# Kernel tuning notes

Hardware: AMD Instinct MI355X
Metric: run time of the kernel (lower is better)

Reference implementation:

```python
import jax, jax.numpy as jnp
import numpy as np


def _knn_idx(pts, k):
    # pts: [N, d] -> indices of k nearest neighbors (incl. self, loop=True) [N, k]
    sq = jnp.sum(pts * pts, axis=-1)
    d2 = sq[:, None] + sq[None, :] - 2.0 * (pts @ pts.T)  # [N, N] squared dists
    _, idx = jax.lax.top_k(-d2, k)  # k smallest distances
    return idx


def _graph_conv(x, nbr, Wr, br, Ws):
    # x: [B, N, d_in], nbr: [B, N, k]. GraphConv (aggr='add'):
    # out_i = W_rel @ sum_j x_j + b_rel + W_root @ x_i
    gathered = jax.vmap(lambda xb, ib: xb[ib])(x, nbr)  # [B, N, k, d_in]
    agg = gathered.sum(axis=2)                          # [B, N, d_in]
    return agg @ Wr.T + br + x @ Ws.T


def setup_inputs() -> dict:
    key = jax.random.key(0)
    ks = jax.random.split(key, 10)
    B, N, D, H = 16, 2048, 3, 128
    s = lambda fi, fo: (2.0 / (fi + fo)) ** 0.5
    return {
        "point_cloud": jax.random.normal(ks[0], (B, N, D), dtype=jnp.float32),
        "W1r": jax.random.normal(ks[1], (H, D), dtype=jnp.float32) * s(D, H),
        "b1": jnp.zeros((H,), dtype=jnp.float32),
        "W1s": jax.random.normal(ks[2], (H, D), dtype=jnp.float32) * s(D, H),
        "W2r": jax.random.normal(ks[3], (H, H), dtype=jnp.float32) * s(H, H),
        "b2": jnp.zeros((H,), dtype=jnp.float32),
        "W2s": jax.random.normal(ks[4], (H, H), dtype=jnp.float32) * s(H, H),
        "W3r": jax.random.normal(ks[5], (H, H), dtype=jnp.float32) * s(H, H),
        "b3": jnp.zeros((H,), dtype=jnp.float32),
        "W3s": jax.random.normal(ks[6], (H, H), dtype=jnp.float32) * s(H, H),
        "k": 16,
    }


def reference(point_cloud, W1r, b1, W1s, W2r, b2, W2s, W3r, b3, W3s, k):
    # knn graph per batch element (loop=True: self-loop included, d(i,i)=0)
    nbr = jax.vmap(lambda p: _knn_idx(p, k))(point_cloud)  # [B, N, k]
    x = jax.nn.relu(_graph_conv(point_cloud, nbr, W1r, b1, W1s))
    x = jax.nn.relu(_graph_conv(x, nbr, W2r, b2, W2s))
    x = _graph_conv(x, nbr, W3r, b3, W3s)
    return x  # [B, N, output_dim]
```

## Files before the change

### kernel.cpp

```cpp
#include <hip/hip_runtime.h>
#include <math.h>

#define NPTS 2048
#define BATCH 16
#define KNN 16
#define HID 128
#define NPOINTS (BATCH * NPTS)
#define RPB 8
#define CAP 64
#define KNN_BLOCKS (NPOINTS / RPB)

typedef __attribute__((ext_vector_type(8))) short bf16x8;
typedef __attribute__((ext_vector_type(4))) float f32x4;

__device__ inline unsigned short f2bf(float f) {
    unsigned u = __float_as_uint(f);
    return (unsigned short)((u + 0x7FFFu + ((u >> 16) & 1u)) >> 16);
}
__device__ inline float bflo(unsigned v) { return __uint_as_float(v << 16); }
__device__ inline float bfhi(unsigned v) { return __uint_as_float(v & 0xFFFF0000u); }


__global__ __launch_bounds__(512) void knn_kernel(
    const float* __restrict__ pc, int* __restrict__ nbr,
    const float* __restrict__ W1r, const float* __restrict__ b1,
    const float* __restrict__ W1s, unsigned short* __restrict__ x1,
    const float* __restrict__ W2r, const float* __restrict__ W2s,
    const float* __restrict__ W3r, const float* __restrict__ W3s,
    unsigned short* __restrict__ wT)
{
    __shared__ __align__(16) float4 pts[NPTS];
    __shared__ unsigned ckey[RPB][CAP];
    __shared__ unsigned cidx[RPB][CAP];
    __shared__ __align__(16) unsigned short xst[RPB][HID];

    if (blockIdx.x >= KNN_BLOCKS) {
        int g = (blockIdx.x - KNN_BLOCKS) * 2048 + (int)threadIdx.x * 4;
        #pragma unroll
        for (int u = 0; u < 4; ++u) {
            int g2 = g + u;
            int mm = g2 >> 14;
            int e = g2 & 16383;
            int r = e >> 7, cch = e & 127;
            const float* s = (mm == 0) ? W2r : (mm == 1) ? W2s
                           : (mm == 2) ? W3r : W3s;
            wT[mm * 16384 + ((cch >> 3) * 128 + r) * 8 + (cch & 7)] = f2bf(s[e]);
        }
        return;
    }

    const int b = blockIdx.x >> 8;
    const int rblk = blockIdx.x & 255;
    const float* p = pc + (size_t)b * NPTS * 3;

    for (int t = threadIdx.x; t < NPTS; t += 512) {
        float x = p[t * 3 + 0], y = p[t * 3 + 1], z = p[t * 3 + 2];
        pts[t] = make_float4(x, y, z, x * x + y * y + z * z);
    }
    __syncthreads();

    const int w = threadIdx.x >> 6;
    const int lane = threadIdx.x & 63;
    const int i = rblk * RPB + w;
    const float4 pi = pts[i];
    const float piw16 = pi.w + 16.0f;

    unsigned key[32];
    unsigned km = 0xFFFFFFFFu;
    #pragma unroll
    for (int t = 0; t < 32; ++t) {
        float4 c = pts[t * 64 + lane];
        float dot = fmaf(pi.x, c.x, fmaf(pi.y, c.y, pi.z * c.z));
        float d2 = fmaf(-2.0f, dot, piw16 + c.w);
        key[t] = __float_as_uint(d2);
        km = min(km, key[t]);
    }

    unsigned v = km;
    #pragma unroll
    for (int k = 2; k <= 64; k <<= 1) {
        #pragma unroll
        for (int j = k >> 1; j > 0; j >>= 1) {
            unsigned o = (unsigned)__shfl_xor((int)v, j, 64);
            bool sel = ((lane & k) == 0) == ((lane & j) == 0);
            v = sel ? min(v, o) : max(v, o);
        }
    }
    const unsigned T0 = (unsigned)__shfl((int)v, 15, 64);

    unsigned base = 0;
    #pragma unroll
    for (int t = 0; t < 32; ++t) {
        bool pred = key[t] <= T0;
        unsigned long long mask = __ballot(pred);
        if (mask) {
            unsigned prefix = __builtin_amdgcn_mbcnt_hi(
                (unsigned)(mask >> 32),
                __builtin_amdgcn_mbcnt_lo((unsigned)mask, 0));
            unsigned pos = base + prefix;
            if (pred && pos < CAP) {
                ckey[w][pos] = key[t];
                cidx[w][pos] = (unsigned)(t * 64 + lane);
            }
            base += (unsigned)__popcll(mask);
        }
    }
    const int m = (int)base;

    int* out = nbr + ((size_t)b * NPTS + i) * KNN;
    float ax = 0.f, ay = 0.f, az = 0.f;

    if (m <= CAP) {
        unsigned k0 = (lane < m) ? ckey[w][lane] : 0xFFFFFFFFu;
        int r0 = 0;
        #pragma unroll 2
        for (int jj = 0; jj < m; ++jj) {
            unsigned kj = ckey[w][jj];
            r0 += (kj < k0) || (kj == k0 && jj < lane);
        }
        if (lane < m && r0 < KNN) {
            unsigned j = cidx[w][lane];
            out[r0] = (int)j;
            float4 q = pts[j]; ax += q.x; ay += q.y; az += q.z;
        }
    } else {
        auto keyat = [&](int t) -> unsigned {
            float4 c = pts[t * 64 + lane];
            float dot = fmaf(pi.x, c.x, fmaf(pi.y, c.y, pi.z * c.z));
            float d2 = fmaf(-2.0f, dot, piw16 + c.w);
            return __float_as_uint(d2);
        };
        unsigned T = 0;
        #pragma unroll 1
        for (int bit = 31; bit >= 0; --bit) {
            unsigned trial = T | (1u << bit);
            int cnt = 0;
            #pragma unroll 1
            for (int t = 0; t < 32; ++t) cnt += (keyat(t) < trial);
            #pragma unroll
            for (int off = 32; off; off >>= 1)
                cnt += __shfl_xor(cnt, off, 64);
            if (cnt < KNN) T = trial;
        }
        unsigned bs = 0;
        #pragma unroll 1
        for (int t = 0; t < 32; ++t) {
            bool p1 = keyat(t) < T;
            unsigned long long mask = __ballot(p1);
            if (mask) {
                unsigned prefix = __builtin_amdgcn_mbcnt_hi(
                    (unsigned)(mask >> 32),
                    __builtin_amdgcn_mbcnt_lo((unsigned)mask, 0));
                if (p1) {
                    out[bs + prefix] = t * 64 + lane;
                    float4 q = pts[t * 64 + lane];
                    ax += q.x; ay += q.y; az += q.z;
                }
                bs += (unsigned)__popcll(mask);
            }
        }
        #pragma unroll 1
        for (int t = 0; t < 32 && bs < KNN; ++t) {
            bool p2 = keyat(t) == T;
            unsigned long long mask = __ballot(p2);
            if (mask) {
                unsigned prefix = __builtin_amdgcn_mbcnt_hi(
                    (unsigned)(mask >> 32),
                    __builtin_amdgcn_mbcnt_lo((unsigned)mask, 0));
                unsigned pos = bs + prefix;
                if (p2 && pos < KNN) {
                    out[pos] = t * 64 + lane;
                    float4 q = pts[t * 64 + lane];
                    ax += q.x; ay += q.y; az += q.z;
                }
                bs += (unsigned)__popcll(mask);
            }
        }
    }

    #pragma unroll
    for (int off = 32; off; off >>= 1) {
        ax += __shfl_xor(ax, off, 64);
        ay += __shfl_xor(ay, off, 64);
        az += __shfl_xor(az, off, 64);
    }

    #pragma unroll
    for (int hh = 0; hh < 2; ++hh) {
        int h = lane + hh * 64;
        float acc = b1[h];
        acc += W1r[h * 3 + 0] * ax + W1r[h * 3 + 1] * ay + W1r[h * 3 + 2] * az;
        acc += W1s[h * 3 + 0] * pi.x + W1s[h * 3 + 1] * pi.y + W1s[h * 3 + 2] * pi.z;
        xst[w][h] = f2bf(fmaxf(acc, 0.f));
    }
    __syncthreads();
    if (threadIdx.x < RPB * 16) {
        int pt = threadIdx.x >> 4, cc = threadIdx.x & 15;
        uint4 vv = *(const uint4*)&xst[pt][cc * 8];
        *(uint4*)&x1[((size_t)b * NPTS + rblk * RPB + pt) * HID + cc * 8] = vv;
    }
}

template <bool RELU, bool OUT_BF16>
__global__ __launch_bounds__(512) void fusedconv_kernel(
    const unsigned short* __restrict__ xR, const int* __restrict__ nbr,
    const unsigned short* __restrict__ wTr, const unsigned short* __restrict__ wTs,
    const float* __restrict__ bias, void* __restrict__ outv)
{
    __shared__ __align__(16) char smem[64 * 132 * 4];
    unsigned short (*agg)[64][8] = (unsigned short (*)[64][8])smem;
    unsigned short (*obf)[136] = (unsigned short (*)[136])smem;
    float (*of32)[132] = (float (*)[132])smem;

    const int p0 = blockIdx.x * 64;
    const int b = blockIdx.x >> 5;
    const unsigned short* xb = xR + (size_t)b * NPTS * HID;

    {
        const int pt = threadIdx.x >> 3;
        const int sub = threadIdx.x & 7;
        const int4* nr4 = (const int4*)(nbr + (size_t)(p0 + pt) * KNN);
        int4 n0 = nr4[0], n1 = nr4[1], n2 = nr4[2], n3 = nr4[3];
        int idx[16] = {n0.x, n0.y, n0.z, n0.w, n1.x, n1.y, n1.z, n1.w,
                       n2.x, n2.y, n2.z, n2.w, n3.x, n3.y, n3.z, n3.w};
        float s0[8] = {0, 0, 0, 0, 0, 0, 0, 0};
        float s1[8] = {0, 0, 0, 0, 0, 0, 0, 0};
        #pragma unroll
        for (int t = 0; t < KNN; ++t) {
            const unsigned short* rowp = xb + (size_t)idx[t] * HID + sub * 8;
            uint4 va = *(const uint4*)rowp;
            uint4 vb = *(const uint4*)(rowp + 64);
            s0[0] += bflo(va.x); s0[1] += bfhi(va.x);
            s0[2] += bflo(va.y); s0[3] += bfhi(va.y);
            s0[4] += bflo(va.z); s0[5] += bfhi(va.z);
            s0[6] += bflo(va.w); s0[7] += bfhi(va.w);
            s1[0] += bflo(vb.x); s1[1] += bfhi(vb.x);
            s1[2] += bflo(vb.y); s1[3] += bfhi(vb.y);
            s1[4] += bflo(vb.z); s1[5] += bfhi(vb.z);
            s1[6] += bflo(vb.w); s1[7] += bfhi(vb.w);
        }
        uint4 o0, o1;
        o0.x = (unsigned)f2bf(s0[0]) | ((unsigned)f2bf(s0[1]) << 16);
        o0.y = (unsigned)f2bf(s0[2]) | ((unsigned)f2bf(s0[3]) << 16);
        o0.z = (unsigned)f2bf(s0[4]) | ((unsigned)f2bf(s0[5]) << 16);
        o0.w = (unsigned)f2bf(s0[6]) | ((unsigned)f2bf(s0[7]) << 16);
        o1.x = (unsigned)f2bf(s1[0]) | ((unsigned)f2bf(s1[1]) << 16);
        o1.y = (unsigned)f2bf(s1[2]) | ((unsigned)f2bf(s1[3]) << 16);
        o1.z = (unsigned)f2bf(s1[4]) | ((unsigned)f2bf(s1[5]) << 16);
        o1.w = (unsigned)f2bf(s1[6]) | ((unsigned)f2bf(s1[7]) << 16);
        *(uint4*)agg[sub][pt] = o0;
        *(uint4*)agg[sub + 8][pt] = o1;
    }
    __syncthreads();

    const int wv = threadIdx.x >> 6;
    const int lane = threadIdx.x & 63;
    const int ptw = (wv & 1) * 32;
    const int h0w = (wv >> 1) * 32;
    const int row = lane & 15;
    const int quad = lane >> 4;

    f32x4 acc[2][2];
    #pragma unroll
    for (int i = 0; i < 2; ++i)
        #pragma unroll
        for (int n = 0; n < 2; ++n) acc[i][n] = (f32x4){0, 0, 0, 0};

    #pragma unroll
    for (int kc = 0; kc < 4; ++kc) {
        const int pl = quad + 4 * kc;
        bf16x8 a0 = *(const bf16x8*)agg[pl][ptw + row];
        bf16x8 a1 = *(const bf16x8*)agg[pl][ptw + 16 + row];
        #pragma unroll
        for (int n = 0; n < 2; ++n) {
            bf16x8 bb = *(const bf16x8*)(wTr + ((size_t)pl * HID + h0w + n * 16 + row) * 8);
            acc[0][n] = __builtin_amdgcn_mfma_f32_16x16x32_bf16(a0, bb, acc[0][n], 0, 0, 0);
            acc[1][n] = __builtin_amdgcn_mfma_f32_16x16x32_bf16(a1, bb, acc[1][n], 0, 0, 0);
        }
    }
    #pragma unroll
    for (int kc = 0; kc < 4; ++kc) {
        const int pl = quad + 4 * kc;
        bf16x8 a0 = *(const bf16x8*)(xR + (size_t)(p0 + ptw + row) * HID + pl * 8);
        bf16x8 a1 = *(const bf16x8*)(xR + (size_t)(p0 + ptw + 16 + row) * HID + pl * 8);
        #pragma unroll
        for (int n = 0; n < 2; ++n) {
            bf16x8 bb = *(const bf16x8*)(wTs + ((size_t)pl * HID + h0w + n * 16 + row) * 8);
            acc[0][n] = __builtin_amdgcn_mfma_f32_16x16x32_bf16(a0, bb, acc[0][n], 0, 0, 0);
            acc[1][n] = __builtin_amdgcn_mfma_f32_16x16x32_bf16(a1, bb, acc[1][n], 0, 0, 0);
        }
    }
    __syncthreads();

    #pragma unroll
    for (int n = 0; n < 2; ++n) {
        float bh = bias[h0w + n * 16 + row];
        #pragma unroll
        for (int i = 0; i < 2; ++i) {
            #pragma unroll
            for (int r = 0; r < 4; ++r) {
                int pt = ptw + i * 16 + quad * 4 + r;
                int hh = h0w + n * 16 + row;
                float vv = acc[i][n][r] + bh;
                if (RELU) vv = fmaxf(vv, 0.f);
                if (OUT_BF16) obf[pt][hh] = f2bf(vv);
                else          of32[pt][hh] = vv;
            }
        }
    }
    __syncthreads();

    if (OUT_BF16) {
        unsigned short* o = (unsigned short*)outv;
        #pragma unroll
        for (int q = 0; q < 2; ++q) {
            int task = q * 512 + threadIdx.x;
            int pt = task >> 4, cc = task & 15;
            *(uint4*)(o + (size_t)(p0 + pt) * HID + cc * 8) =
                *(const uint4*)&obf[pt][cc * 8];
        }
    } else {
        float* o = (float*)outv;
        #pragma unroll
        for (int q = 0; q < 4; ++q) {
            int task = q * 512 + threadIdx.x;
            int rr = task >> 5, ch = task & 31;
            *(float4*)(o + (size_t)(p0 + rr) * HID + ch * 4) =
                *(const float4*)&of32[rr][ch * 4];
        }
    }
}

extern "C" void kernel_launch(void* const* d_in, const int* in_sizes, int n_in,
                              void* d_out, int out_size, void* d_ws, size_t ws_size,
                              hipStream_t stream)
{
    const float* pc  = (const float*)d_in[0];
    const float* W1r = (const float*)d_in[1];
    const float* b1  = (const float*)d_in[2];
    const float* W1s = (const float*)d_in[3];
    const float* W2r = (const float*)d_in[4];
    const float* b2  = (const float*)d_in[5];
    const float* W2s = (const float*)d_in[6];
    const float* W3r = (const float*)d_in[7];
    const float* b3  = (const float*)d_in[8];
    const float* W3s = (const float*)d_in[9];
    float* out = (float*)d_out;

    char* ws = (char*)d_ws;
    const size_t MB = 1024 * 1024;
    const size_t XSZ = (size_t)NPOINTS * HID * 2;
    int*            nbr  = (int*)ws;
    unsigned short* x1   = (unsigned short*)(ws + 2 * MB);
    unsigned short* x2   = (unsigned short*)(ws + 2 * MB + XSZ);
    unsigned short* wT   = (unsigned short*)(ws + 2 * MB + 2 * XSZ);
    unsigned short* w2rT = wT;
    unsigned short* w2sT = wT + 16384;
    unsigned short* w3rT = wT + 32768;
    unsigned short* w3sT = wT + 49152;

    knn_kernel<<<KNN_BLOCKS + 32, 512, 0, stream>>>(
        pc, nbr, W1r, b1, W1s, x1, W2r, W2s, W3r, W3s, wT);

    fusedconv_kernel<true, true><<<NPOINTS / 64, 512, 0, stream>>>(
        x1, nbr, w2rT, w2sT, b2, x2);

    fusedconv_kernel<false, false><<<NPOINTS / 64, 512, 0, stream>>>(
        x2, nbr, w3rT, w3sT, b3, out);
}
```

Baseline: 156.6 us.

## Process two query points per wavefront in KNN kernel with packed candidates

Each wavefront now handles two query points, so each shared-memory load of a candidate point is reused for two distance computations, and the number of KNN blocks is halved (fewer redundant point-cloud loads into LDS). Candidate key and index are packed into one 64-bit value, so ranking needs a single comparison and one LDS array. This doubles the key registers per thread (64 instead of 32), which can cut occupancy or cause spills, and halves the block count.

```diff
diff --git a/kernel.cpp b/kernel.cpp
--- a/kernel.cpp
+++ b/kernel.cpp
@@ -6,9 +6,9 @@
 #define KNN 16
 #define HID 128
 #define NPOINTS (BATCH * NPTS)
-#define RPB 8
+#define QPB 16
 #define CAP 64
-#define KNN_BLOCKS (NPOINTS / RPB)
+#define KNN_BLOCKS (NPOINTS / QPB)
 
 typedef __attribute__((ext_vector_type(8))) short bf16x8;
 typedef __attribute__((ext_vector_type(4))) float f32x4;
@@ -30,9 +30,8 @@
     unsigned short* __restrict__ wT)
 {
     __shared__ __align__(16) float4 pts[NPTS];
-    __shared__ unsigned ckey[RPB][CAP];
-    __shared__ unsigned cidx[RPB][CAP];
-    __shared__ __align__(16) unsigned short xst[RPB][HID];
+    __shared__ unsigned long long cand[QPB][CAP];
+    __shared__ __align__(16) unsigned short xst[QPB][HID];
 
     if (blockIdx.x >= KNN_BLOCKS) {
         int g = (blockIdx.x - KNN_BLOCKS) * 2048 + (int)threadIdx.x * 4;
@@ -49,8 +48,8 @@
         return;
     }
 
-    const int b = blockIdx.x >> 8;
-    const int rblk = blockIdx.x & 255;
+    const int b = blockIdx.x >> 7;
+    const int rblk = blockIdx.x & 127;
     const float* p = pc + (size_t)b * NPTS * 3;
 
     for (int t = threadIdx.x; t < NPTS; t += 512) {
@@ -61,74 +60,92 @@
 
     const int w = threadIdx.x >> 6;
     const int lane = threadIdx.x & 63;
-    const int i = rblk * RPB + w;
-    const float4 pi = pts[i];
-    const float piw16 = pi.w + 16.0f;
-
-    unsigned key[32];
-    unsigned km = 0xFFFFFFFFu;
+    const int r0q = w * 2, r1q = w * 2 + 1;
+    const int i0 = rblk * QPB + r0q, i1 = i0 + 1;
+    const float4 pi0 = pts[i0];
+    const float4 pi1 = pts[i1];
+    const float p0w16 = pi0.w + 16.0f;
+    const float p1w16 = pi1.w + 16.0f;
+
+    unsigned key0[32], key1[32];
+    unsigned km0 = 0xFFFFFFFFu, km1 = 0xFFFFFFFFu;
     #pragma unroll
     for (int t = 0; t < 32; ++t) {
         float4 c = pts[t * 64 + lane];
-        float dot = fmaf(pi.x, c.x, fmaf(pi.y, c.y, pi.z * c.z));
-        float d2 = fmaf(-2.0f, dot, piw16 + c.w);
-        key[t] = __float_as_uint(d2);
-        km = min(km, key[t]);
-    }
-
-    unsigned v = km;
+        float dot0 = fmaf(pi0.x, c.x, fmaf(pi0.y, c.y, pi0.z * c.z));
+        float dot1 = fmaf(pi1.x, c.x, fmaf(pi1.y, c.y, pi1.z * c.z));
+        key0[t] = __float_as_uint(fmaf(-2.0f, dot0, p0w16 + c.w));
+        key1[t] = __float_as_uint(fmaf(-2.0f, dot1, p1w16 + c.w));
+        km0 = min(km0, key0[t]);
+        km1 = min(km1, key1[t]);
+    }
+
+    unsigned v0 = km0, v1 = km1;
     #pragma unroll
     for (int k = 2; k <= 64; k <<= 1) {
         #pragma unroll
         for (int j = k >> 1; j > 0; j >>= 1) {
-            unsigned o = (unsigned)__shfl_xor((int)v, j, 64);
+            unsigned o0 = (unsigned)__shfl_xor((int)v0, j, 64);
+            unsigned o1 = (unsigned)__shfl_xor((int)v1, j, 64);
             bool sel = ((lane & k) == 0) == ((lane & j) == 0);
-            v = sel ? min(v, o) : max(v, o);
-        }
-    }
-    const unsigned T0 = (unsigned)__shfl((int)v, 15, 64);
-
-    unsigned base = 0;
+            v0 = sel ? min(v0, o0) : max(v0, o0);
+            v1 = sel ? min(v1, o1) : max(v1, o1);
+        }
+    }
+    const unsigned T00 = (unsigned)__shfl((int)v0, 15, 64);
+    const unsigned T01 = (unsigned)__shfl((int)v1, 15, 64);
+
+    unsigned base0 = 0, base1 = 0;
     #pragma unroll
     for (int t = 0; t < 32; ++t) {
-        bool pred = key[t] <= T0;
-        unsigned long long mask = __ballot(pred);
-        if (mask) {
-            unsigned prefix = __builtin_amdgcn_mbcnt_hi(
-                (unsigned)(mask >> 32),
-                __builtin_amdgcn_mbcnt_lo((unsigned)mask, 0));
-            unsigned pos = base + prefix;
-            if (pred && pos < CAP) {
-                ckey[w][pos] = key[t];
-                cidx[w][pos] = (unsigned)(t * 64 + lane);
-            }
-            base += (unsigned)__popcll(mask);
-        }
-    }
-    const int m = (int)base;
-
-    int* out = nbr + ((size_t)b * NPTS + i) * KNN;
-    float ax = 0.f, ay = 0.f, az = 0.f;
-
-    if (m <= CAP) {
-        unsigned k0 = (lane < m) ? ckey[w][lane] : 0xFFFFFFFFu;
-        int r0 = 0;
+        bool pr0 = key0[t] <= T00;
+        unsigned long long mk0 = __ballot(pr0);
+        if (mk0) {
+            unsigned pf = __builtin_amdgcn_mbcnt_hi(
+                (unsigned)(mk0 >> 32),
+                __builtin_amdgcn_mbcnt_lo((unsigned)mk0, 0));
+            unsigned pos = base0 + pf;
+            if (pr0 && pos < CAP)
+                cand[r0q][pos] = ((unsigned long long)key0[t] << 32)
+                               | (unsigned)(t * 64 + lane);
+            base0 += (unsigned)__popcll(mk0);
+        }
+        bool pr1 = key1[t] <= T01;
+        unsigned long long mk1 = __ballot(pr1);
+        if (mk1) {
+            unsigned pf = __builtin_amdgcn_mbcnt_hi(
+                (unsigned)(mk1 >> 32),
+                __builtin_amdgcn_mbcnt_lo((unsigned)mk1, 0));
+            unsigned pos = base1 + pf;
+            if (pr1 && pos < CAP)
+                cand[r1q][pos] = ((unsigned long long)key1[t] << 32)
+                               | (unsigned)(t * 64 + lane);
+            base1 += (unsigned)__popcll(mk1);
+        }
+    }
+    const int m0 = (int)base0, m1 = (int)base1;
+
+    int* out0 = nbr + ((size_t)b * NPTS + i0) * KNN;
+    int* out1 = nbr + ((size_t)b * NPTS + i1) * KNN;
+    float ax0 = 0.f, ay0 = 0.f, az0 = 0.f;
+    float ax1 = 0.f, ay1 = 0.f, az1 = 0.f;
+
+    if (m0 <= CAP) {
+        unsigned long long c0 = (lane < m0) ? cand[r0q][lane] : ~0ULL;
+        int rk = 0;
         #pragma unroll 2
-        for (int jj = 0; jj < m; ++jj) {
-            unsigned kj = ckey[w][jj];
-            r0 += (kj < k0) || (kj == k0 && jj < lane);
-        }
-        if (lane < m && r0 < KNN) {
-            unsigned j = cidx[w][lane];
-            out[r0] = (int)j;
-            float4 q = pts[j]; ax += q.x; ay += q.y; az += q.z;
+        for (int jj = 0; jj < m0; ++jj)
+            rk += (cand[r0q][jj] < c0);
+        if (lane < m0 && rk < KNN) {
+            unsigned j = (unsigned)c0;
+            out0[rk] = (int)j;
+            float4 q = pts[j]; ax0 += q.x; ay0 += q.y; az0 += q.z;
         }
     } else {
         auto keyat = [&](int t) -> unsigned {
             float4 c = pts[t * 64 + lane];
-            float dot = fmaf(pi.x, c.x, fmaf(pi.y, c.y, pi.z * c.z));
-            float d2 = fmaf(-2.0f, dot, piw16 + c.w);
-            return __float_as_uint(d2);
+            float dot = fmaf(pi0.x, c.x, fmaf(pi0.y, c.y, pi0.z * c.z));
+            return __float_as_uint(fmaf(-2.0f, dot, p0w16 + c.w));
         };
         unsigned T = 0;
         #pragma unroll 1
@@ -138,8 +155,7 @@
             #pragma unroll 1
             for (int t = 0; t < 32; ++t) cnt += (keyat(t) < trial);
             #pragma unroll
-            for (int off = 32; off; off >>= 1)
-                cnt += __shfl_xor(cnt, off, 64);
+            for (int off = 32; off; off >>= 1) cnt += __shfl_xor(cnt, off, 64);
             if (cnt < KNN) T = trial;
         }
         unsigned bs = 0;
@@ -148,13 +164,13 @@
             bool p1 = keyat(t) < T;
             unsigned long long mask = __ballot(p1);
             if (mask) {
-                unsigned prefix = __builtin_amdgcn_mbcnt_hi(
+                unsigned pf = __builtin_amdgcn_mbcnt_hi(
                     (unsigned)(mask >> 32),
                     __builtin_amdgcn_mbcnt_lo((unsigned)mask, 0));
                 if (p1) {
-                    out[bs + prefix] = t * 64 + lane;
+                    out0[bs + pf] = t * 64 + lane;
                     float4 q = pts[t * 64 + lane];
-                    ax += q.x; ay += q.y; az += q.z;
+                    ax0 += q.x; ay0 += q.y; az0 += q.z;
                 }
                 bs += (unsigned)__popcll(mask);
             }
@@ -164,40 +180,112 @@
             bool p2 = keyat(t) == T;
             unsigned long long mask = __ballot(p2);
             if (mask) {
-                unsigned prefix = __builtin_amdgcn_mbcnt_hi(
+                unsigned pf = __builtin_amdgcn_mbcnt_hi(
                     (unsigned)(mask >> 32),
                     __builtin_amdgcn_mbcnt_lo((unsigned)mask, 0));
-                unsigned pos = bs + prefix;
+                unsigned pos = bs + pf;
                 if (p2 && pos < KNN) {
-                    out[pos] = t * 64 + lane;
+                    out0[pos] = t * 64 + lane;
                     float4 q = pts[t * 64 + lane];
-                    ax += q.x; ay += q.y; az += q.z;
+                    ax0 += q.x; ay0 += q.y; az0 += q.z;
                 }
                 bs += (unsigned)__popcll(mask);
             }
         }
     }
 
+    if (m1 <= CAP) {
+        unsigned long long c1 = (lane < m1) ? cand[r1q][lane] : ~0ULL;
+        int rk = 0;
+        #pragma unroll 2
+        for (int jj = 0; jj < m1; ++jj)
+            rk += (cand[r1q][jj] < c1);
+        if (lane < m1 && rk < KNN) {
+            unsigned j = (unsigned)c1;
+            out1[rk] = (int)j;
+            float4 q = pts[j]; ax1 += q.x; ay1 += q.y; az1 += q.z;
+        }
+    } else {
+        auto keyat = [&](int t) -> unsigned {
+            float4 c = pts[t * 64 + lane];
+            float dot = fmaf(pi1.x, c.x, fmaf(pi1.y, c.y, pi1.z * c.z));
+            return __float_as_uint(fmaf(-2.0f, dot, p1w16 + c.w));
+        };
+        unsigned T = 0;
+        #pragma unroll 1
+        for (int bit = 31; bit >= 0; --bit) {
+            unsigned trial = T | (1u << bit);
+            int cnt = 0;
+            #pragma unroll 1
+            for (int t = 0; t < 32; ++t) cnt += (keyat(t) < trial);
+            #pragma unroll
+            for (int off = 32; off; off >>= 1) cnt += __shfl_xor(cnt, off, 64);
+            if (cnt < KNN) T = trial;
+        }
+        unsigned bs = 0;
+        #pragma unroll 1
+        for (int t = 0; t < 32; ++t) {
+            bool p1 = keyat(t) < T;
+            unsigned long long mask = __ballot(p1);
+            if (mask) {
+                unsigned pf = __builtin_amdgcn_mbcnt_hi(
+                    (unsigned)(mask >> 32),
+                    __builtin_amdgcn_mbcnt_lo((unsigned)mask, 0));
+                if (p1) {
+                    out1[bs + pf] = t * 64 + lane;
+                    float4 q = pts[t * 64 + lane];
+                    ax1 += q.x; ay1 += q.y; az1 += q.z;
+                }
+                bs += (unsigned)__popcll(mask);
+            }
+        }
+        #pragma unroll 1
+        for (int t = 0; t < 32 && bs < KNN; ++t) {
+            bool p2 = keyat(t) == T;
+            unsigned long long mask = __ballot(p2);
+            if (mask) {
+                unsigned pf = __builtin_amdgcn_mbcnt_hi(
+                    (unsigned)(mask >> 32),
+                    __builtin_amdgcn_mbcnt_lo((unsigned)mask, 0));
+                unsigned pos = bs + pf;
+                if (p2 && pos < KNN) {
+                    out1[pos] = t * 64 + lane;
+                    float4 q = pts[t * 64 + lane];
+                    ax1 += q.x; ay1 += q.y; az1 += q.z;
+                }
+                bs += (unsigned)__popcll(mask);
+            }
+        }
+    }
+
     #pragma unroll
     for (int off = 32; off; off >>= 1) {
-        ax += __shfl_xor(ax, off, 64);
-        ay += __shfl_xor(ay, off, 64);
-        az += __shfl_xor(az, off, 64);
+        ax0 += __shfl_xor(ax0, off, 64);
+        ay0 += __shfl_xor(ay0, off, 64);
+        az0 += __shfl_xor(az0, off, 64);
+        ax1 += __shfl_xor(ax1, off, 64);
+        ay1 += __shfl_xor(ay1, off, 64);
+        az1 += __shfl_xor(az1, off, 64);
     }
 
     #pragma unroll
     for (int hh = 0; hh < 2; ++hh) {
         int h = lane + hh * 64;
-        float acc = b1[h];
-        acc += W1r[h * 3 + 0] * ax + W1r[h * 3 + 1] * ay + W1r[h * 3 + 2] * az;
-        acc += W1s[h * 3 + 0] * pi.x + W1s[h * 3 + 1] * pi.y + W1s[h * 3 + 2] * pi.z;
-        xst[w][h] = f2bf(fmaxf(acc, 0.f));
+        float w0 = W1r[h * 3 + 0], w1 = W1r[h * 3 + 1], w2 = W1r[h * 3 + 2];
+        float s0 = W1s[h * 3 + 0], s1 = W1s[h * 3 + 1], s2 = W1s[h * 3 + 2];
+        float bb = b1[h];
+        float a0 = bb + w0 * ax0 + w1 * ay0 + w2 * az0
+                      + s0 * pi0.x + s1 * pi0.y + s2 * pi0.z;
+        float a1 = bb + w0 * ax1 + w1 * ay1 + w2 * az1
+                      + s0 * pi1.x + s1 * pi1.y + s2 * pi1.z;
+        xst[r0q][h] = f2bf(fmaxf(a0, 0.f));
+        xst[r1q][h] = f2bf(fmaxf(a1, 0.f));
     }
     __syncthreads();
-    if (threadIdx.x < RPB * 16) {
+    if (threadIdx.x < QPB * 16) {
         int pt = threadIdx.x >> 4, cc = threadIdx.x & 15;
         uint4 vv = *(const uint4*)&xst[pt][cc * 8];
-        *(uint4*)&x1[((size_t)b * NPTS + rblk * RPB + pt) * HID + cc * 8] = vv;
+        *(uint4*)&x1[((size_t)b * NPTS + rblk * QPB + pt) * HID + cc * 8] = vv;
     }
 }
 
```

Result: slower. 187.2 us (+19.5%).
